# Kernel tuning notes

Measured on AMD Instinct MI355X. Metric: run time of the kernel, lower is better.

## Reference

```python
import jax, jax.numpy as jnp
import numpy as np

N_NODES = 100000
N_EDGES = 1600000
K = 3


def _cheb_conv(x, row, col, w, W, b):
    # SpMM: out[row] += w * x[col]
    def spmm(v):
        return jax.ops.segment_sum(w[:, None] * v[col], row, num_segments=N_NODES)
    Ts = [x, spmm(x)]
    for _ in range(2, K):
        Ts.append(2.0 * spmm(Ts[-1]) - Ts[-2])
    return jnp.concatenate(Ts, axis=-1) @ W.T + b


def setup_inputs() -> dict:
    key = jax.random.key(0)
    ks = jax.random.split(key, 12)
    inp = {
        "x": jax.random.normal(ks[0], (N_NODES, 128), dtype=jnp.float32),
        "edge_index": jax.random.randint(ks[1], (2, N_EDGES), 0, N_NODES, dtype=jnp.int32),
        "edge_weight": jax.random.normal(ks[2], (N_EDGES,), dtype=jnp.float32) * 0.05,
        "W_in": jax.random.normal(ks[3], (128, K * 128), dtype=jnp.float32) * (1.0 / np.sqrt(K * 128)),
        "b_in": jnp.zeros((128,), dtype=jnp.float32),
        "W_h1": jax.random.normal(ks[4], (128, K * 128), dtype=jnp.float32) * (1.0 / np.sqrt(K * 128)),
        "b_h1": jnp.zeros((128,), dtype=jnp.float32),
        "W_h2": jax.random.normal(ks[5], (128, K * 128), dtype=jnp.float32) * (1.0 / np.sqrt(K * 128)),
        "b_h2": jnp.zeros((128,), dtype=jnp.float32),
        "W_out": jax.random.normal(ks[6], (64, K * 128), dtype=jnp.float32) * (1.0 / np.sqrt(K * 128)),
        "b_out": jnp.zeros((64,), dtype=jnp.float32),
    }
    return inp


def reference(x, edge_index, edge_weight, W_in, b_in, W_h1, b_h1, W_h2, b_h2, W_out, b_out):
    row, col = edge_index[0], edge_index[1]
    # dropout is inactive at inference (training=False)
    h = jax.nn.relu(_cheb_conv(x, row, col, edge_weight, W_in, b_in))
    for (W, b) in ((W_h1, b_h1), (W_h2, b_h2)):
        h = jax.nn.relu(_cheb_conv(h, row, col, edge_weight, W, b) + h)  # residual
    out = _cheb_conv(h, row, col, edge_weight, W_out, b_out)
    return out
```

## Files before the change

kernel.cpp:

```cpp
#include <hip/hip_runtime.h>
#include <hip/hip_bf16.h>
#include <stdint.h>
#include <stddef.h>

#define N_NODES 100000
#define N_EDGES 1600000
#define FEAT 128
#define NB_SCAN ((N_NODES + 255) / 256)
#define LDS_PITCH 136
#define CAP 24
#define NL (CAP / 4)
#define NBKT ((N_NODES + 255) / 256)
#define BCAP 8160
#define EPB 2048

typedef __attribute__((ext_vector_type(8))) short bf16x8;
typedef __attribute__((ext_vector_type(4))) float f32x4;
typedef unsigned short u16;

__device__ __forceinline__ float bf2f(u16 u) {
    union { unsigned int i; float f; } v; v.i = ((unsigned int)u) << 16; return v.f;
}
__device__ __forceinline__ u16 f2bf(float f) {
    union { float f; unsigned int i; } v; v.f = f;
    unsigned int x = v.i;
    return (u16)((x + 0x7fffu + ((x >> 16) & 1u)) >> 16);
}


__global__ void hist_kernel(const int* __restrict__ rows, int* __restrict__ counts) {
    int e = blockIdx.x * blockDim.x + threadIdx.x;
    if (e < N_EDGES) {
        int r = rows[e];
        r = min(max(r, 0), N_NODES - 1);
        atomicAdd(&counts[r], 1);
    }
}

__global__ void reduce_counts_kernel(const int* __restrict__ counts, int* __restrict__ bsum) {
    __shared__ int s[256];
    int i = blockIdx.x * 256 + threadIdx.x;
    int v = (i < N_NODES) ? counts[i] : 0;
    s[threadIdx.x] = v; __syncthreads();
    for (int off = 128; off > 0; off >>= 1) {
        if (threadIdx.x < off) s[threadIdx.x] += s[threadIdx.x + off];
        __syncthreads();
    }
    if (threadIdx.x == 0) bsum[blockIdx.x] = s[0];
}

__global__ void scan_bsums_kernel(int* __restrict__ bsum, int* __restrict__ row_ptr) {
    __shared__ int s[512];
    int t = threadIdx.x;
    int v = (t < NB_SCAN) ? bsum[t] : 0;
    s[t] = v; __syncthreads();
    for (int off = 1; off < 512; off <<= 1) {
        int x = (t >= off) ? s[t - off] : 0;
        __syncthreads();
        s[t] += x;
        __syncthreads();
    }
    if (t < NB_SCAN) bsum[t] = s[t] - v;
    if (t == NB_SCAN - 1) row_ptr[N_NODES] = s[t];
}

__global__ void write_rowptr_kernel(int* __restrict__ counts, const int* __restrict__ bsum,
                                    int* __restrict__ row_ptr) {
    __shared__ int s[256];
    int i = blockIdx.x * 256 + threadIdx.x;
    int v = (i < N_NODES) ? counts[i] : 0;
    s[threadIdx.x] = v; __syncthreads();
    for (int off = 1; off < 256; off <<= 1) {
        int x = (threadIdx.x >= off) ? s[threadIdx.x - off] : 0;
        __syncthreads();
        s[threadIdx.x] += x;
        __syncthreads();
    }
    if (i < N_NODES) {
        row_ptr[i] = bsum[blockIdx.x] + s[threadIdx.x] - v;
        counts[i] = 0;
    }
}

__global__ void scatter_kernel(const int* __restrict__ rows, const int* __restrict__ cols,
                               const float* __restrict__ w, const int* __restrict__ row_ptr,
                               int* __restrict__ fill, int2* __restrict__ ecw) {
    int e = blockIdx.x * blockDim.x + threadIdx.x;
    if (e < N_EDGES) {
        int r = rows[e];
        r = min(max(r, 0), N_NODES - 1);
        int pos = row_ptr[r] + atomicAdd(&fill[r], 1);
        pos = min(max(pos, 0), N_EDGES - 1);
        int c = cols[e];
        c = min(max(c, 0), N_NODES - 1);
        ecw[pos] = make_int2(c, __float_as_int(w[e]));
    }
}


__global__ __launch_bounds__(256) void bucket_p1_kernel(const int* __restrict__ rows,
                                                        const int* __restrict__ cols,
                                                        const float* __restrict__ w,
                                                        int* __restrict__ gcnt,
                                                        int2* __restrict__ bbuf) {
    __shared__ int s_cnt[NBKT];
    __shared__ int s_base[NBKT];
    int tid = threadIdx.x;
    for (int b = tid; b < NBKT; b += 256) s_cnt[b] = 0;
    __syncthreads();
    int e0 = blockIdx.x * EPB;
#pragma unroll
    for (int it = 0; it < EPB / 256; ++it) {
        int e = e0 + it * 256 + tid;
        if (e < N_EDGES) {
            int r = min(max(rows[e], 0), N_NODES - 1);
            atomicAdd(&s_cnt[r >> 8], 1);
        }
    }
    __syncthreads();
    for (int b = tid; b < NBKT; b += 256) {
        s_base[b] = atomicAdd(&gcnt[b], s_cnt[b]);
        s_cnt[b] = 0;
    }
    __syncthreads();
#pragma unroll
    for (int it = 0; it < EPB / 256; ++it) {
        int e = e0 + it * 256 + tid;
        if (e < N_EDGES) {
            int r = min(max(rows[e], 0), N_NODES - 1);
            int b = r >> 8;
            int k = atomicAdd(&s_cnt[b], 1);
            int pos = min(s_base[b] + k, BCAP - 1);
            int c = min(max(cols[e], 0), N_NODES - 1);
            bbuf[(size_t)b * BCAP + pos] = make_int2(c | ((r & 255) << 20), __float_as_int(w[e]));
        }
    }
}

__global__ __launch_bounds__(256) void bucket_count_kernel(const int* __restrict__ gcnt,
                                                           const int2* __restrict__ bbuf,
                                                           int* __restrict__ counts) {
    __shared__ int s_cnt[256];
    int b = blockIdx.x, tid = threadIdx.x;
    s_cnt[tid] = 0; __syncthreads();
    int cnt = min(gcnt[b], BCAP);
    for (int i = tid; i < cnt; i += 256)
        atomicAdd(&s_cnt[bbuf[(size_t)b * BCAP + i].x >> 20], 1);
    __syncthreads();
    int r = b * 256 + tid;
    if (r < N_NODES) counts[r] = s_cnt[tid];
}

__global__ __launch_bounds__(256) void bucket_scatter_kernel(const int* __restrict__ gcnt,
                                                             const int2* __restrict__ bbuf,
                                                             const int* __restrict__ row_ptr,
                                                             int2* __restrict__ ecw) {
    __shared__ int s_fill[256];
    int b = blockIdx.x, tid = threadIdx.x;
    s_fill[tid] = 0; __syncthreads();
    int cnt = min(gcnt[b], BCAP);
    for (int i = tid; i < cnt; i += 256) {
        int2 p = bbuf[(size_t)b * BCAP + i];
        int rl = p.x >> 20;
        int r = b * 256 + rl;
        int pos = row_ptr[r] + atomicAdd(&s_fill[rl], 1);
        pos = min(max(pos, 0), N_EDGES - 1);
        ecw[pos] = make_int2(p.x & 0xFFFFF, p.y);
    }
}

__device__ __forceinline__ float w_fold(const float* W, int o, int k) {
    if (k < 128)      return W[o * 384 + k] - W[o * 384 + 256 + k];
    else if (k < 256) return W[o * 384 + k];
    else              return 2.0f * W[o * 384 + k];
}

__global__ void prep_w_kernel(const float* __restrict__ W, u16* __restrict__ Wp, int O) {
    int i = blockIdx.x * blockDim.x + threadIdx.x;
    if (i >= O * 384) return;
    int o = i / 384, k = i % 384;
    Wp[i] = f2bf(w_fold(W, o, k));
}

__global__ void prep_w2_kernel(const float* __restrict__ W, u16* __restrict__ Wp2, int O) {
    int i = blockIdx.x * blockDim.x + threadIdx.x;
    int total = (O / 16) * 12 * 64;
    if (i >= total) return;
    int ot = i / 768;
    int rem = i % 768;
    int kk = rem / 64;
    int l = rem % 64;
    int q = l >> 4, r = l & 15;
    int o = ot * 16 + r;
    int kbase = kk * 32 + q * 8;
#pragma unroll
    for (int j = 0; j < 8; ++j)
        Wp2[(size_t)i * 8 + j] = f2bf(w_fold(W, o, kbase + j));
}


__global__ void cvt_kernel(const float* __restrict__ x, u16* __restrict__ y) {
    int i = blockIdx.x * blockDim.x + threadIdx.x;
    if (i >= N_NODES * FEAT / 4) return;
    float4 v = ((const float4*)x)[i];
    ushort4 o;
    o.x = f2bf(v.x); o.y = f2bf(v.y); o.z = f2bf(v.z); o.w = f2bf(v.w);
    ((ushort4*)y)[i] = o;
}


__device__ __forceinline__ void load_meta(const int2* __restrict__ ecw, int s, int n,
                                          int lane, int& call, float& wall) {
    int idx = s + max(0, min(lane, n - 1));
    idx = min(idx, N_EDGES - 1);
    int2 cw = ecw[idx];
    call = cw.x;
    wall = (lane < n) ? __int_as_float(cw.y) : 0.f;
}

__device__ __forceinline__ void issue_row(const u16* __restrict__ X, int call,
                                          int g, int f, bf16x8* q) {
#pragma unroll
    for (int k = 0; k < NL; ++k) {
        int col = __shfl(call, k * 4 + g);
        q[k] = *(const bf16x8*)(X + (size_t)col * FEAT + f * 8);
    }
}

__device__ __forceinline__ void reduce_row(const bf16x8* q, float wall,
                                           int g, float* acc) {
#pragma unroll
    for (int k = 0; k < NL; ++k) {
        float wj = __shfl(wall, k * 4 + g);
#pragma unroll
        for (int j = 0; j < 8; ++j) acc[j] += wj * bf2f((u16)q[k][j]);
    }
}


__global__ __launch_bounds__(256) void spmm1_kernel(const int* __restrict__ row_ptr,
                                                    const int2* __restrict__ ecw,
                                                    const u16* __restrict__ X,
                                                    u16* __restrict__ Y) {
    int lane = threadIdx.x & 63;
    int g = lane >> 4, f = lane & 15;
    int rr = (blockIdx.x * blockDim.x + threadIdx.x) >> 6;

    int s = row_ptr[rr], e = row_ptr[rr + 1];
    float acc[8];
#pragma unroll
    for (int j = 0; j < 8; ++j) acc[j] = 0.f;

    {
        int call; float wall;
        load_meta(ecw, s, min(e - s, CAP), lane, call, wall);
        bf16x8 q[NL];
        issue_row(X, call, g, f, q);
        reduce_row(q, wall, g, acc);
    }
    for (int cs = s + CAP; cs < e; cs += CAP) {
        int c2; float w2;
        load_meta(ecw, cs, min(e - cs, CAP), lane, c2, w2);
        bf16x8 qt[NL];
        issue_row(X, c2, g, f, qt);
        reduce_row(qt, w2, g, acc);
    }

#pragma unroll
    for (int j = 0; j < 8; ++j) {
        acc[j] += __shfl_xor(acc[j], 16);
        acc[j] += __shfl_xor(acc[j], 32);
    }
    if (g == 0) {
        u16 tmp[8];
#pragma unroll
        for (int j = 0; j < 8; ++j) tmp[j] = f2bf(acc[j]);
        *(bf16x8*)(Y + (size_t)rr * FEAT + f * 8) = *(const bf16x8*)tmp;
    }
}


__device__ __forceinline__ void gather4(const int* __restrict__ row_ptr,
                                        const int2* __restrict__ ecw,
                                        const u16* __restrict__ X,
                                        int r0, int lane, int g, int f,
                                        float acc[4][8]) {
    int s[4], e[4];
    int call[4]; float wall[4];
#pragma unroll
    for (int y = 0; y < 4; ++y) {
        s[y] = row_ptr[r0 + y];
        e[y] = row_ptr[r0 + y + 1];
    }
#pragma unroll
    for (int y = 0; y < 4; ++y)
        load_meta(ecw, s[y], min(e[y] - s[y], CAP), lane, call[y], wall[y]);
#pragma unroll
    for (int y = 0; y < 4; ++y)
#pragma unroll
        for (int j = 0; j < 8; ++j) acc[y][j] = 0.f;

    bf16x8 q0[NL], q1[NL], q2[NL], q3[NL];
    issue_row(X, call[0], g, f, q0);
    issue_row(X, call[1], g, f, q1);
    reduce_row(q0, wall[0], g, acc[0]);
    issue_row(X, call[2], g, f, q2);
    reduce_row(q1, wall[1], g, acc[1]);
    issue_row(X, call[3], g, f, q3);
    reduce_row(q2, wall[2], g, acc[2]);
    reduce_row(q3, wall[3], g, acc[3]);

#pragma unroll
    for (int y = 0; y < 4; ++y) {
        for (int cs = s[y] + CAP; cs < e[y]; cs += CAP) {
            int c2; float w2;
            load_meta(ecw, cs, min(e[y] - cs, CAP), lane, c2, w2);
            bf16x8 qt[NL];
            issue_row(X, c2, g, f, qt);
            reduce_row(qt, w2, g, acc[y]);
        }
    }

#pragma unroll
    for (int y = 0; y < 4; ++y)
#pragma unroll
        for (int j = 0; j < 8; ++j) {
            acc[y][j] += __shfl_xor(acc[y][j], 16);
            acc[y][j] += __shfl_xor(acc[y][j], 32);
        }
}

__global__ __launch_bounds__(256) void spmm_kernel(const int* __restrict__ row_ptr,
                                                   const int2* __restrict__ ecw,
                                                   const u16* __restrict__ X,
                                                   u16* __restrict__ Y) {
    int wid = threadIdx.x >> 6;
    int lane = threadIdx.x & 63;
    int g = lane >> 4, f = lane & 15;
    int r0 = blockIdx.x * 16 + wid * 4;

    float acc[4][8];
    gather4(row_ptr, ecw, X, r0, lane, g, f, acc);

    if (g == 0) {
#pragma unroll
        for (int y = 0; y < 4; ++y) {
            u16 tmp[8];
#pragma unroll
            for (int j = 0; j < 8; ++j) tmp[j] = f2bf(acc[y][j]);
            *(bf16x8*)(Y + (size_t)(r0 + y) * FEAT + f * 8) = *(const bf16x8*)tmp;
        }
    }
}


template <int O, bool RELU, bool RES, bool OUT_F32>
__global__ __launch_bounds__(256) void gemm_kernel(const u16* __restrict__ H,
                                                   const u16* __restrict__ T1,
                                                   const u16* __restrict__ S2,
                                                   const u16* __restrict__ Wp2,
                                                   const float* __restrict__ bias,
                                                   void* __restrict__ outv) {
    __shared__ __align__(16) u16 sA[3][32][LDS_PITCH];
    int tid = threadIdx.x;
    int m0 = blockIdx.x * 32;

#pragma unroll
    for (int p = 0; p < 3; ++p) {
        const u16* sp = (p == 0) ? H : (p == 1) ? T1 : S2;
#pragma unroll
        for (int u = 0; u < 2; ++u) {
            int unit = u * 256 + tid;
            int row = unit >> 4, seg = unit & 15;
            *(bf16x8*)&sA[p][row][seg * 8] =
                *(const bf16x8*)(sp + (size_t)(m0 + row) * FEAT + seg * 8);
        }
    }
    __syncthreads();

    int lane = tid & 63, wid = tid >> 6;
    int r = lane & 15, q = lane >> 4;
    constexpr int NW = O / 64;
    f32x4 acc0[NW], acc1[NW];
#pragma unroll
    for (int t = 0; t < NW; ++t) {
        acc0[t] = (f32x4){0.f, 0.f, 0.f, 0.f};
        acc1[t] = (f32x4){0.f, 0.f, 0.f, 0.f};
    }

#pragma unroll
    for (int kk = 0; kk < 12; ++kk) {
        int p = kk >> 2, ko = kk & 3;
        bf16x8 af0 = *(const bf16x8*)&sA[p][r][ko * 32 + q * 8];
        bf16x8 af1 = *(const bf16x8*)&sA[p][16 + r][ko * 32 + q * 8];
#pragma unroll
        for (int t = 0; t < NW; ++t) {
            int ot = wid * NW + t;
            bf16x8 bfr = *(const bf16x8*)(Wp2 + ((size_t)(ot * 12 + kk) * 64 + lane) * 8);
            acc0[t] = __builtin_amdgcn_mfma_f32_16x16x32_bf16(af0, bfr, acc0[t], 0, 0, 0);
            acc1[t] = __builtin_amdgcn_mfma_f32_16x16x32_bf16(af1, bfr, acc1[t], 0, 0, 0);
        }
    }

#pragma unroll
    for (int t = 0; t < NW; ++t) {
        int col = (wid * NW + t) * 16 + r;
        float bv = bias[col];
#pragma unroll
        for (int i = 0; i < 4; ++i) {
            int lrow = q * 4 + i;
            float v0 = acc0[t][i] + bv;
            if (RES)  v0 += bf2f(sA[0][lrow][col]);
            if (RELU) v0 = fmaxf(v0, 0.f);
            float v1 = acc1[t][i] + bv;
            if (RES)  v1 += bf2f(sA[0][16 + lrow][col]);
            if (RELU) v1 = fmaxf(v1, 0.f);
            if (OUT_F32) {
                ((float*)outv)[(size_t)(m0 + lrow) * O + col] = v0;
                ((float*)outv)[(size_t)(m0 + 16 + lrow) * O + col] = v1;
            } else {
                ((u16*)outv)[(size_t)(m0 + lrow) * O + col] = f2bf(v0);
                ((u16*)outv)[(size_t)(m0 + 16 + lrow) * O + col] = f2bf(v1);
            }
        }
    }
}


template <int O, bool RELU, bool RES, bool OUT_F32>
__global__ __launch_bounds__(256) void fused_gemm_kernel(const int* __restrict__ row_ptr,
                                                         const int2* __restrict__ ecw,
                                                         const u16* __restrict__ H,
                                                         const u16* __restrict__ T1,
                                                         const u16* __restrict__ Wp,
                                                         const float* __restrict__ bias,
                                                         void* __restrict__ outv) {
    __shared__ __align__(16) u16 sT[16 * LDS_PITCH];
    int wid = threadIdx.x >> 6;
    int lane = threadIdx.x & 63;
    int g = lane >> 4, f = lane & 15;
    int m0 = blockIdx.x * 16;

    {
        float acc[4][8];
        gather4(row_ptr, ecw, T1, m0 + wid * 4, lane, g, f, acc);
        if (g == 0) {
#pragma unroll
            for (int y = 0; y < 4; ++y) {
                u16 tmp[8];
#pragma unroll
                for (int j = 0; j < 8; ++j) tmp[j] = f2bf(acc[y][j]);
                *(bf16x8*)(sT + (wid * 4 + y) * LDS_PITCH + f * 8) = *(const bf16x8*)tmp;
            }
        }
    }
    __syncthreads();

    int r = f, q = g;
    constexpr int NT = O / 16;
    constexpr int NW = NT / 4;
    f32x4 acc[NW];
#pragma unroll
    for (int t = 0; t < NW; ++t) acc[t] = (f32x4){0.f, 0.f, 0.f, 0.f};

#pragma unroll
    for (int kk = 0; kk < 12; ++kk) {
        bf16x8 af;
        if (kk < 4)
            af = *(const bf16x8*)(H + (size_t)(m0 + r) * FEAT + kk * 32 + q * 8);
        else if (kk < 8)
            af = *(const bf16x8*)(T1 + (size_t)(m0 + r) * FEAT + (kk - 4) * 32 + q * 8);
        else
            af = *(const bf16x8*)(sT + r * LDS_PITCH + (kk - 8) * 32 + q * 8);
#pragma unroll
        for (int t = 0; t < NW; ++t) {
            int ot = wid * NW + t;
            bf16x8 bfr = *(const bf16x8*)(Wp + (size_t)(ot * 16 + r) * 384 + kk * 32 + q * 8);
            acc[t] = __builtin_amdgcn_mfma_f32_16x16x32_bf16(af, bfr, acc[t], 0, 0, 0);
        }
    }

#pragma unroll
    for (int t = 0; t < NW; ++t) {
        int col = (wid * NW + t) * 16 + r;
        float bv = bias[col];
#pragma unroll
        for (int i = 0; i < 4; ++i) {
            int row = m0 + q * 4 + i;
            float v = acc[t][i] + bv;
            if (RES)  v += bf2f(H[(size_t)row * FEAT + col]);
            if (RELU) v = fmaxf(v, 0.f);
            if (OUT_F32) ((float*)outv)[(size_t)row * O + col] = v;
            else         ((u16*)outv)[(size_t)row * O + col] = f2bf(v);
        }
    }
}


static inline size_t align_up(size_t x) { return (x + 255) & ~(size_t)255; }

extern "C" void kernel_launch(void* const* d_in, const int* in_sizes, int n_in,
                              void* d_out, int out_size, void* d_ws, size_t ws_size,
                              hipStream_t stream) {
    const float* x     = (const float*)d_in[0];
    const int*   ei    = (const int*)d_in[1];
    const float* ew    = (const float*)d_in[2];
    const float* W_in  = (const float*)d_in[3];
    const float* b_in  = (const float*)d_in[4];
    const float* W_h1  = (const float*)d_in[5];
    const float* b_h1  = (const float*)d_in[6];
    const float* W_h2  = (const float*)d_in[7];
    const float* b_h2  = (const float*)d_in[8];
    const float* W_out = (const float*)d_in[9];
    const float* b_out = (const float*)d_in[10];

    const int* rows = ei;
    const int* cols = ei + N_EDGES;

    char* w = (char*)d_ws;
    size_t off = 0;
    int* counts = (int*)(w + off);            off = align_up(off + (size_t)N_NODES * 4);
    int* row_ptr= (int*)(w + off);            off = align_up(off + (size_t)(N_NODES + 1) * 4);
    int* bsum   = (int*)(w + off);            off = align_up(off + 512 * 4);
    int2* ecw   = (int2*)(w + off);           off = align_up(off + (size_t)N_EDGES * 8);
    u16* t1     = (u16*)(w + off);            off = align_up(off + (size_t)N_NODES * FEAT * 2);
    u16* h      = (u16*)(w + off);            off = align_up(off + (size_t)N_NODES * FEAT * 2);
    u16* Wp_in  = (u16*)(w + off);            off = align_up(off + (size_t)128 * 384 * 2);
    u16* Wp_h1  = (u16*)(w + off);            off = align_up(off + (size_t)128 * 384 * 2);
    u16* Wp_h2  = (u16*)(w + off);            off = align_up(off + (size_t)128 * 384 * 2);
    u16* Wp_out = (u16*)(w + off);            off = align_up(off + (size_t)64 * 384 * 2);
    u16* s2     = (u16*)(w + off);            size_t off2 = align_up(off + (size_t)N_NODES * FEAT * 2);
    u16* W2_in  = (u16*)(w + off2);           off2 = align_up(off2 + (size_t)128 * 384 * 2);
    u16* W2_h1  = (u16*)(w + off2);           off2 = align_up(off2 + (size_t)128 * 384 * 2);
    u16* W2_h2  = (u16*)(w + off2);           off2 = align_up(off2 + (size_t)128 * 384 * 2);
    u16* W2_out = (u16*)(w + off2);           off2 = align_up(off2 + (size_t)64 * 384 * 2);
    int* gcnt   = (int*)(w + off2);           off2 = align_up(off2 + (size_t)NBKT * 4);
    const bool use_split = (ws_size >= off2);
    static_assert((size_t)NBKT * BCAP * 8 <= (size_t)N_NODES * FEAT * 2, "bucket buffer exceeds s2");

    hipMemsetAsync(counts, 0, (size_t)N_NODES * 4, stream);

    cvt_kernel<<<(N_NODES * FEAT / 4 + 255) / 256, 256, 0, stream>>>(x, h);

    const int grid16 = N_NODES / 16;
    const int grid32 = N_NODES / 32;
    const int grid1  = N_NODES * 64 / 256;

    if (use_split) {
        hipMemsetAsync(gcnt, 0, (size_t)NBKT * 4, stream);
        int2* bbuf = (int2*)s2;
        bucket_p1_kernel<<<(N_EDGES + EPB - 1) / EPB, 256, 0, stream>>>(rows, cols, ew, gcnt, bbuf);
        bucket_count_kernel<<<NBKT, 256, 0, stream>>>(gcnt, bbuf, counts);
        reduce_counts_kernel<<<NB_SCAN, 256, 0, stream>>>(counts, bsum);
        scan_bsums_kernel<<<1, 512, 0, stream>>>(bsum, row_ptr);
        write_rowptr_kernel<<<NB_SCAN, 256, 0, stream>>>(counts, bsum, row_ptr);
        bucket_scatter_kernel<<<NBKT, 256, 0, stream>>>(gcnt, bbuf, row_ptr, ecw);

        prep_w2_kernel<<<(128 * 384 / 8 + 255) / 256, 256, 0, stream>>>(W_in, W2_in, 128);
        prep_w2_kernel<<<(128 * 384 / 8 + 255) / 256, 256, 0, stream>>>(W_h1, W2_h1, 128);
        prep_w2_kernel<<<(128 * 384 / 8 + 255) / 256, 256, 0, stream>>>(W_h2, W2_h2, 128);
        prep_w2_kernel<<<(64 * 384 / 8 + 255) / 256, 256, 0, stream>>>(W_out, W2_out, 64);

        spmm1_kernel<<<grid1, 256, 0, stream>>>(row_ptr, ecw, h, t1);
        spmm1_kernel<<<grid1, 256, 0, stream>>>(row_ptr, ecw, t1, s2);
        gemm_kernel<128, true, false, false><<<grid32, 256, 0, stream>>>(h, t1, s2, W2_in, b_in, h);
        spmm1_kernel<<<grid1, 256, 0, stream>>>(row_ptr, ecw, h, t1);
        spmm1_kernel<<<grid1, 256, 0, stream>>>(row_ptr, ecw, t1, s2);
        gemm_kernel<128, true, true, false><<<grid32, 256, 0, stream>>>(h, t1, s2, W2_h1, b_h1, h);
        spmm1_kernel<<<grid1, 256, 0, stream>>>(row_ptr, ecw, h, t1);
        spmm1_kernel<<<grid1, 256, 0, stream>>>(row_ptr, ecw, t1, s2);
        gemm_kernel<128, true, true, false><<<grid32, 256, 0, stream>>>(h, t1, s2, W2_h2, b_h2, h);
        spmm1_kernel<<<grid1, 256, 0, stream>>>(row_ptr, ecw, h, t1);
        spmm1_kernel<<<grid1, 256, 0, stream>>>(row_ptr, ecw, t1, s2);
        gemm_kernel<64, false, false, true><<<grid32, 256, 0, stream>>>(h, t1, s2, W2_out, b_out, d_out);
    } else {
        hist_kernel<<<N_EDGES / 256, 256, 0, stream>>>(rows, counts);
        reduce_counts_kernel<<<NB_SCAN, 256, 0, stream>>>(counts, bsum);
        scan_bsums_kernel<<<1, 512, 0, stream>>>(bsum, row_ptr);
        write_rowptr_kernel<<<NB_SCAN, 256, 0, stream>>>(counts, bsum, row_ptr);
        scatter_kernel<<<N_EDGES / 256, 256, 0, stream>>>(rows, cols, ew, row_ptr, counts, ecw);

        prep_w_kernel<<<(128 * 384 + 255) / 256, 256, 0, stream>>>(W_in, Wp_in, 128);
        prep_w_kernel<<<(128 * 384 + 255) / 256, 256, 0, stream>>>(W_h1, Wp_h1, 128);
        prep_w_kernel<<<(128 * 384 + 255) / 256, 256, 0, stream>>>(W_h2, Wp_h2, 128);
        prep_w_kernel<<<(64 * 384 + 255) / 256, 256, 0, stream>>>(W_out, Wp_out, 64);

        spmm_kernel<<<grid16, 256, 0, stream>>>(row_ptr, ecw, h, t1);
        fused_gemm_kernel<128, true, false, false><<<grid16, 256, 0, stream>>>(
            row_ptr, ecw, h, t1, Wp_in, b_in, h);
        spmm_kernel<<<grid16, 256, 0, stream>>>(row_ptr, ecw, h, t1);
        fused_gemm_kernel<128, true, true, false><<<grid16, 256, 0, stream>>>(
            row_ptr, ecw, h, t1, Wp_h1, b_h1, h);
        spmm_kernel<<<grid16, 256, 0, stream>>>(row_ptr, ecw, h, t1);
        fused_gemm_kernel<128, true, true, false><<<grid16, 256, 0, stream>>>(
            row_ptr, ecw, h, t1, Wp_h2, b_h2, h);
        spmm_kernel<<<grid16, 256, 0, stream>>>(row_ptr, ecw, h, t1);
        fused_gemm_kernel<64, false, false, true><<<grid16, 256, 0, stream>>>(
            row_ptr, ecw, h, t1, Wp_out, b_out, d_out);
    }
}
```

Measured before the change: 748.7 us.

## Process two rows per wave in SpMM and use 64-row GEMM tiles

The SpMM kernel now has each wavefront handle two consecutive rows, issuing both rows' gathers before reducing them, which raises memory-level parallelism per wave. The GEMM kernel tile grows from 32 to 64 rows, so each weight fragment loaded from global memory feeds four MFMAs instead of two. A clamped load and a bounds check on stores handle the partial last tile. In exchange, register and LDS use per block go up, which may lower occupancy.

```diff
diff --git a/kernel.cpp b/kernel.cpp
--- a/kernel.cpp
+++ b/kernel.cpp
@@ -238,44 +238,60 @@
 }
 
 
-__global__ __launch_bounds__(256) void spmm1_kernel(const int* __restrict__ row_ptr,
+__global__ __launch_bounds__(256) void spmm2_kernel(const int* __restrict__ row_ptr,
                                                     const int2* __restrict__ ecw,
                                                     const u16* __restrict__ X,
                                                     u16* __restrict__ Y) {
     int lane = threadIdx.x & 63;
     int g = lane >> 4, f = lane & 15;
-    int rr = (blockIdx.x * blockDim.x + threadIdx.x) >> 6;
-
-    int s = row_ptr[rr], e = row_ptr[rr + 1];
-    float acc[8];
-#pragma unroll
-    for (int j = 0; j < 8; ++j) acc[j] = 0.f;
-
-    {
-        int call; float wall;
-        load_meta(ecw, s, min(e - s, CAP), lane, call, wall);
-        bf16x8 q[NL];
-        issue_row(X, call, g, f, q);
-        reduce_row(q, wall, g, acc);
-    }
-    for (int cs = s + CAP; cs < e; cs += CAP) {
+    int r0 = ((blockIdx.x * blockDim.x + threadIdx.x) >> 6) * 2;
+
+    int s0 = row_ptr[r0], m = row_ptr[r0 + 1], e1 = row_ptr[r0 + 2];
+    float acc0[8], acc1[8];
+#pragma unroll
+    for (int j = 0; j < 8; ++j) { acc0[j] = 0.f; acc1[j] = 0.f; }
+
+    int call0, call1; float wall0, wall1;
+    load_meta(ecw, s0, min(m - s0, CAP), lane, call0, wall0);
+    load_meta(ecw, m, min(e1 - m, CAP), lane, call1, wall1);
+    bf16x8 q0[NL], q1[NL];
+    issue_row(X, call0, g, f, q0);
+    issue_row(X, call1, g, f, q1);
+    reduce_row(q0, wall0, g, acc0);
+    reduce_row(q1, wall1, g, acc1);
+
+    for (int cs = s0 + CAP; cs < m; cs += CAP) {
         int c2; float w2;
-        load_meta(ecw, cs, min(e - cs, CAP), lane, c2, w2);
+        load_meta(ecw, cs, min(m - cs, CAP), lane, c2, w2);
         bf16x8 qt[NL];
         issue_row(X, c2, g, f, qt);
-        reduce_row(qt, w2, g, acc);
+        reduce_row(qt, w2, g, acc0);
+    }
+    for (int cs = m + CAP; cs < e1; cs += CAP) {
+        int c2; float w2;
+        load_meta(ecw, cs, min(e1 - cs, CAP), lane, c2, w2);
+        bf16x8 qt[NL];
+        issue_row(X, c2, g, f, qt);
+        reduce_row(qt, w2, g, acc1);
     }
 
 #pragma unroll
     for (int j = 0; j < 8; ++j) {
-        acc[j] += __shfl_xor(acc[j], 16);
-        acc[j] += __shfl_xor(acc[j], 32);
+        acc0[j] += __shfl_xor(acc0[j], 16);
+        acc0[j] += __shfl_xor(acc0[j], 32);
+        acc1[j] += __shfl_xor(acc1[j], 16);
+        acc1[j] += __shfl_xor(acc1[j], 32);
     }
     if (g == 0) {
         u16 tmp[8];
 #pragma unroll
-        for (int j = 0; j < 8; ++j) tmp[j] = f2bf(acc[j]);
-        *(bf16x8*)(Y + (size_t)rr * FEAT + f * 8) = *(const bf16x8*)tmp;
+        for (int j = 0; j < 8; ++j) tmp[j] = f2bf(acc0[j]);
+        *(bf16x8*)(Y + (size_t)r0 * FEAT + f * 8) = *(const bf16x8*)tmp;
+    } else if (g == 1) {
+        u16 tmp[8];
+#pragma unroll
+        for (int j = 0; j < 8; ++j) tmp[j] = f2bf(acc1[j]);
+        *(bf16x8*)(Y + (size_t)(r0 + 1) * FEAT + f * 8) = *(const bf16x8*)tmp;
     }
 }
 
@@ -361,19 +377,20 @@
                                                    const u16* __restrict__ Wp2,
                                                    const float* __restrict__ bias,
                                                    void* __restrict__ outv) {
-    __shared__ __align__(16) u16 sA[3][32][LDS_PITCH];
+    __shared__ __align__(16) u16 sA[3][64][LDS_PITCH];
     int tid = threadIdx.x;
-    int m0 = blockIdx.x * 32;
+    int m0 = blockIdx.x * 64;
 
 #pragma unroll
     for (int p = 0; p < 3; ++p) {
         const u16* sp = (p == 0) ? H : (p == 1) ? T1 : S2;
 #pragma unroll
-        for (int u = 0; u < 2; ++u) {
+        for (int u = 0; u < 4; ++u) {
             int unit = u * 256 + tid;
             int row = unit >> 4, seg = unit & 15;
+            int srow = min(m0 + row, N_NODES - 1);
             *(bf16x8*)&sA[p][row][seg * 8] =
-                *(const bf16x8*)(sp + (size_t)(m0 + row) * FEAT + seg * 8);
+                *(const bf16x8*)(sp + (size_t)srow * FEAT + seg * 8);
         }
     }
     __syncthreads();
@@ -381,24 +398,27 @@
     int lane = tid & 63, wid = tid >> 6;
     int r = lane & 15, q = lane >> 4;
     constexpr int NW = O / 64;
-    f32x4 acc0[NW], acc1[NW];
-#pragma unroll
-    for (int t = 0; t < NW; ++t) {
-        acc0[t] = (f32x4){0.f, 0.f, 0.f, 0.f};
-        acc1[t] = (f32x4){0.f, 0.f, 0.f, 0.f};
-    }
+    f32x4 acc[NW][4];
+#pragma unroll
+    for (int t = 0; t < NW; ++t)
+#pragma unroll
+        for (int sub = 0; sub < 4; ++sub)
+            acc[t][sub] = (f32x4){0.f, 0.f, 0.f, 0.f};
 
 #pragma unroll
     for (int kk = 0; kk < 12; ++kk) {
         int p = kk >> 2, ko = kk & 3;
-        bf16x8 af0 = *(const bf16x8*)&sA[p][r][ko * 32 + q * 8];
-        bf16x8 af1 = *(const bf16x8*)&sA[p][16 + r][ko * 32 + q * 8];
+        bf16x8 af[4];
+#pragma unroll
+        for (int sub = 0; sub < 4; ++sub)
+            af[sub] = *(const bf16x8*)&sA[p][sub * 16 + r][ko * 32 + q * 8];
 #pragma unroll
         for (int t = 0; t < NW; ++t) {
             int ot = wid * NW + t;
             bf16x8 bfr = *(const bf16x8*)(Wp2 + ((size_t)(ot * 12 + kk) * 64 + lane) * 8);
-            acc0[t] = __builtin_amdgcn_mfma_f32_16x16x32_bf16(af0, bfr, acc0[t], 0, 0, 0);
-            acc1[t] = __builtin_amdgcn_mfma_f32_16x16x32_bf16(af1, bfr, acc1[t], 0, 0, 0);
+#pragma unroll
+            for (int sub = 0; sub < 4; ++sub)
+                acc[t][sub] = __builtin_amdgcn_mfma_f32_16x16x32_bf16(af[sub], bfr, acc[t][sub], 0, 0, 0);
         }
     }
 
@@ -407,20 +427,18 @@
         int col = (wid * NW + t) * 16 + r;
         float bv = bias[col];
 #pragma unroll
-        for (int i = 0; i < 4; ++i) {
-            int lrow = q * 4 + i;
-            float v0 = acc0[t][i] + bv;
-            if (RES)  v0 += bf2f(sA[0][lrow][col]);
-            if (RELU) v0 = fmaxf(v0, 0.f);
-            float v1 = acc1[t][i] + bv;
-            if (RES)  v1 += bf2f(sA[0][16 + lrow][col]);
-            if (RELU) v1 = fmaxf(v1, 0.f);
-            if (OUT_F32) {
-                ((float*)outv)[(size_t)(m0 + lrow) * O + col] = v0;
-                ((float*)outv)[(size_t)(m0 + 16 + lrow) * O + col] = v1;
-            } else {
-                ((u16*)outv)[(size_t)(m0 + lrow) * O + col] = f2bf(v0);
-                ((u16*)outv)[(size_t)(m0 + 16 + lrow) * O + col] = f2bf(v1);
+        for (int sub = 0; sub < 4; ++sub) {
+#pragma unroll
+            for (int i = 0; i < 4; ++i) {
+                int lrow = sub * 16 + q * 4 + i;
+                int row = m0 + lrow;
+                if (row < N_NODES) {
+                    float v = acc[t][sub][i] + bv;
+                    if (RES)  v += bf2f(sA[0][lrow][col]);
+                    if (RELU) v = fmaxf(v, 0.f);
+                    if (OUT_F32) ((float*)outv)[(size_t)row * O + col] = v;
+                    else         ((u16*)outv)[(size_t)row * O + col] = f2bf(v);
+                }
             }
         }
     }
@@ -543,8 +561,8 @@
     cvt_kernel<<<(N_NODES * FEAT / 4 + 255) / 256, 256, 0, stream>>>(x, h);
 
     const int grid16 = N_NODES / 16;
-    const int grid32 = N_NODES / 32;
-    const int grid1  = N_NODES * 64 / 256;
+    const int grid64 = (N_NODES + 63) / 64;
+    const int grid2  = N_NODES / 2 * 64 / 256;
 
     if (use_split) {
         hipMemsetAsync(gcnt, 0, (size_t)NBKT * 4, stream);
@@ -561,18 +579,18 @@
         prep_w2_kernel<<<(128 * 384 / 8 + 255) / 256, 256, 0, stream>>>(W_h2, W2_h2, 128);
         prep_w2_kernel<<<(64 * 384 / 8 + 255) / 256, 256, 0, stream>>>(W_out, W2_out, 64);
 
-        spmm1_kernel<<<grid1, 256, 0, stream>>>(row_ptr, ecw, h, t1);
-        spmm1_kernel<<<grid1, 256, 0, stream>>>(row_ptr, ecw, t1, s2);
-        gemm_kernel<128, true, false, false><<<grid32, 256, 0, stream>>>(h, t1, s2, W2_in, b_in, h);
-        spmm1_kernel<<<grid1, 256, 0, stream>>>(row_ptr, ecw, h, t1);
-        spmm1_kernel<<<grid1, 256, 0, stream>>>(row_ptr, ecw, t1, s2);
-        gemm_kernel<128, true, true, false><<<grid32, 256, 0, stream>>>(h, t1, s2, W2_h1, b_h1, h);
-        spmm1_kernel<<<grid1, 256, 0, stream>>>(row_ptr, ecw, h, t1);
-        spmm1_kernel<<<grid1, 256, 0, stream>>>(row_ptr, ecw, t1, s2);
-        gemm_kernel<128, true, true, false><<<grid32, 256, 0, stream>>>(h, t1, s2, W2_h2, b_h2, h);
-        spmm1_kernel<<<grid1, 256, 0, stream>>>(row_ptr, ecw, h, t1);
-        spmm1_kernel<<<grid1, 256, 0, stream>>>(row_ptr, ecw, t1, s2);
-        gemm_kernel<64, false, false, true><<<grid32, 256, 0, stream>>>(h, t1, s2, W2_out, b_out, d_out);
+        spmm2_kernel<<<grid2, 256, 0, stream>>>(row_ptr, ecw, h, t1);
+        spmm2_kernel<<<grid2, 256, 0, stream>>>(row_ptr, ecw, t1, s2);
+        gemm_kernel<128, true, false, false><<<grid64, 256, 0, stream>>>(h, t1, s2, W2_in, b_in, h);
+        spmm2_kernel<<<grid2, 256, 0, stream>>>(row_ptr, ecw, h, t1);
+        spmm2_kernel<<<grid2, 256, 0, stream>>>(row_ptr, ecw, t1, s2);
+        gemm_kernel<128, true, true, false><<<grid64, 256, 0, stream>>>(h, t1, s2, W2_h1, b_h1, h);
+        spmm2_kernel<<<grid2, 256, 0, stream>>>(row_ptr, ecw, h, t1);
+        spmm2_kernel<<<grid2, 256, 0, stream>>>(row_ptr, ecw, t1, s2);
+        gemm_kernel<128, true, true, false><<<grid64, 256, 0, stream>>>(h, t1, s2, W2_h2, b_h2, h);
+        spmm2_kernel<<<grid2, 256, 0, stream>>>(row_ptr, ecw, h, t1);
+        spmm2_kernel<<<grid2, 256, 0, stream>>>(row_ptr, ecw, t1, s2);
+        gemm_kernel<64, false, false, true><<<grid64, 256, 0, stream>>>(h, t1, s2, W2_out, b_out, d_out);
     } else {
         hist_kernel<<<N_EDGES / 256, 256, 0, stream>>>(rows, counts);
         reduce_counts_kernel<<<NB_SCAN, 256, 0, stream>>>(counts, bsum);
```

Result: slower. 787.7 us (+5.2%).
